# Optimization experiments

Hardware: AMD Instinct MI355X
Metric: run time of the kernel (lower is better)

## Reference

```python
import jax, jax.numpy as jnp
import numpy as np

EPS = 1e-4  # matches torch: x.norm(2, dim=1, keepdim=True) + 0.0001

def setup_inputs() -> dict:
    key = jax.random.key(0)
    k1, k2, k3 = jax.random.split(key, 3)
    B, IN, OUT = 16384, 2048, 2048
    x = jax.random.normal(k1, (B, IN), dtype=jnp.float32)
    # nn.Linear default init: U(-1/sqrt(in), 1/sqrt(in))
    bound = 1.0 / np.sqrt(IN)
    W = jax.random.uniform(k2, (OUT, IN), dtype=jnp.float32, minval=-bound, maxval=bound)
    b = jax.random.uniform(k3, (OUT,), dtype=jnp.float32, minval=-bound, maxval=bound)
    return {"x": x, "W": W, "b": b}

def reference(x, W, b):
    # L2-normalize each row, then Linear, then ReLU
    norm = jnp.linalg.norm(x, ord=2, axis=1, keepdims=True)  # [B, 1]
    x_dir = x / (norm + EPS)
    h = jnp.einsum('bi,oi->bo', x_dir, W) + b  # [B, OUT]
    return jax.nn.relu(h)
```

## Files before the change

kernel.cpp:

```cpp
#include <hip/hip_runtime.h>
#include <hip/hip_bf16.h>
#include <stdint.h>

#define B_ROWS 16384
#define IN_DIM 2048
#define OUT_DIM 2048

typedef __attribute__((ext_vector_type(4))) float f32x4;
typedef __attribute__((ext_vector_type(8))) short s16x8;

__device__ __forceinline__ unsigned short f2bf_rne(float f) {
  union { float f; unsigned u; } c; c.f = f;
  unsigned u = c.u;
  return (unsigned short)((u + 0x7FFFu + ((u >> 16) & 1u)) >> 16);
}

#define PREP_X_BLOCKS 4096
#define PREP_W_BLOCKS 2048

__global__ void __launch_bounds__(256) prep_kernel(const float* __restrict__ x,
                                                   unsigned short* __restrict__ xn,
                                                   float* __restrict__ scale,
                                                   const float* __restrict__ W,
                                                   unsigned short* __restrict__ Wb) {
  if (blockIdx.x < PREP_X_BLOCKS) {
    const int row  = (blockIdx.x * 256 + threadIdx.x) >> 6;
    const int lane = threadIdx.x & 63;
    const float4* xr = (const float4*)(x + (size_t)row * IN_DIM);
    unsigned short* xrow = xn + (size_t)row * IN_DIM;

    float ss = 0.0f;
    #pragma unroll
    for (int j = 0; j < 4; ++j) {
      const int f4 = j * 128 + lane * 2;
      float4 v0 = xr[f4 + 0];
      float4 v1 = xr[f4 + 1];
      ss += v0.x * v0.x + v0.y * v0.y + v0.z * v0.z + v0.w * v0.w +
            v1.x * v1.x + v1.y * v1.y + v1.z * v1.z + v1.w * v1.w;
      s16x8 p;
      p[0] = (short)f2bf_rne(v0.x); p[1] = (short)f2bf_rne(v0.y);
      p[2] = (short)f2bf_rne(v0.z); p[3] = (short)f2bf_rne(v0.w);
      p[4] = (short)f2bf_rne(v1.x); p[5] = (short)f2bf_rne(v1.y);
      p[6] = (short)f2bf_rne(v1.z); p[7] = (short)f2bf_rne(v1.w);
      *(s16x8*)(xrow + f4 * 4) = p;
    }

    #pragma unroll
    for (int m = 32; m > 0; m >>= 1) ss += __shfl_xor(ss, m, 64);
    if (lane == 0) scale[row] = 1.0f / (sqrtf(ss) + 1e-4f);
  } else {
    const size_t base = (size_t)(blockIdx.x - PREP_X_BLOCKS) * 2048 +
                        (size_t)threadIdx.x * 8;
    const float4* wp = (const float4*)(W + base);
    float4 v0 = wp[0];
    float4 v1 = wp[1];
    s16x8 p;
    p[0] = (short)f2bf_rne(v0.x); p[1] = (short)f2bf_rne(v0.y);
    p[2] = (short)f2bf_rne(v0.z); p[3] = (short)f2bf_rne(v0.w);
    p[4] = (short)f2bf_rne(v1.x); p[5] = (short)f2bf_rne(v1.y);
    p[6] = (short)f2bf_rne(v1.z); p[7] = (short)f2bf_rne(v1.w);
    *(s16x8*)(Wb + base) = p;
  }
}

__global__ void __launch_bounds__(256) gemm_kernel(const unsigned short* __restrict__ A,
                                                   const unsigned short* __restrict__ Bm,
                                                   const float* __restrict__ scale,
                                                   const float* __restrict__ bias,
                                                   float* __restrict__ out) {
  constexpr int BK = 64;
  __shared__ short As[128 * BK];
  __shared__ short Bs[128 * BK];

  const int tid = threadIdx.x;
  const int bid   = blockIdx.x;
  const int group = bid >> 7;
  const int w_    = bid & 127;
  const int bm    = group * 8 + (w_ & 7);
  const int bn    = w_ >> 3;

  const int lane = tid & 63;
  const int wave = tid >> 6;
  const int wm   = wave >> 1;
  const int wn   = wave & 1;
  const int lrow = lane & 15;
  const int lq   = lane >> 4;

  const int ar = tid >> 3;
  const int ac = ((tid & 7) ^ (ar & 7)) * 8;
  const unsigned short* ag = A  + (size_t)(bm * 128 + ar) * IN_DIM + ac;
  const unsigned short* bg = Bm + (size_t)(bn * 128 + ar) * IN_DIM + ac;
  char* asl = (char*)As + tid * 16;
  char* bsl = (char*)Bs + tid * 16;

  f32x4 acc[4][4] = {};

  for (int k0 = 0; k0 < IN_DIM; k0 += BK) {
    #pragma unroll
    for (int i = 0; i < 4; ++i) {
      __builtin_amdgcn_global_load_lds(
          (const __attribute__((address_space(1))) unsigned int*)(ag + (size_t)i * 32 * IN_DIM),
          (__attribute__((address_space(3))) unsigned int*)(asl + i * 4096), 16, 0, 0);
    }
    #pragma unroll
    for (int i = 0; i < 4; ++i) {
      __builtin_amdgcn_global_load_lds(
          (const __attribute__((address_space(1))) unsigned int*)(bg + (size_t)i * 32 * IN_DIM),
          (__attribute__((address_space(3))) unsigned int*)(bsl + i * 4096), 16, 0, 0);
    }
    ag += BK;
    bg += BK;
    __syncthreads();

    #pragma unroll
    for (int kk = 0; kk < 2; ++kk) {
      s16x8 af[4], bf[4];
      #pragma unroll
      for (int mi = 0; mi < 4; ++mi) {
        const int R = wm * 64 + mi * 16 + lrow;
        af[mi] = *(const s16x8*)(As + R * BK + (((kk * 4 + lq) ^ (lrow & 7)) * 8));
      }
      #pragma unroll
      for (int ni = 0; ni < 4; ++ni) {
        const int R = wn * 64 + ni * 16 + lrow;
        bf[ni] = *(const s16x8*)(Bs + R * BK + (((kk * 4 + lq) ^ (lrow & 7)) * 8));
      }
      #pragma unroll
      for (int mi = 0; mi < 4; ++mi)
        #pragma unroll
        for (int ni = 0; ni < 4; ++ni)
          acc[mi][ni] = __builtin_amdgcn_mfma_f32_16x16x32_bf16(af[mi], bf[ni], acc[mi][ni], 0, 0, 0);
    }
    __syncthreads();
  }

  const int row0 = bm * 128 + wm * 64 + lq * 4;
  const int col0 = bn * 128 + wn * 64 + lrow;
  #pragma unroll
  for (int mi = 0; mi < 4; ++mi) {
    const int row = row0 + mi * 16;
    const f32x4 sc = *(const f32x4*)(scale + row);
    #pragma unroll
    for (int ni = 0; ni < 4; ++ni) {
      const int col = col0 + ni * 16;
      const float bcol = bias[col];
      #pragma unroll
      for (int r = 0; r < 4; ++r) {
        float v = acc[mi][ni][r] * sc[r] + bcol;
        out[(size_t)(row + r) * OUT_DIM + col] = fmaxf(v, 0.0f);
      }
    }
  }
}

extern "C" void kernel_launch(void* const* d_in, const int* in_sizes, int n_in,
                              void* d_out, int out_size, void* d_ws, size_t ws_size,
                              hipStream_t stream) {
  const float* x = (const float*)d_in[0];
  const float* W = (const float*)d_in[1];
  const float* b = (const float*)d_in[2];
  float* out = (float*)d_out;

  char* ws = (char*)d_ws;
  unsigned short* xn    = (unsigned short*)ws;
  unsigned short* Wb    = (unsigned short*)(ws + (size_t)67108864);
  float*          scale = (float*)(ws + (size_t)67108864 + (size_t)8388608);

  prep_kernel<<<PREP_X_BLOCKS + PREP_W_BLOCKS, 256, 0, stream>>>(x, xn, scale, W, Wb);

  gemm_kernel<<<(OUT_DIM / 128) * (B_ROWS / 128), 256, 0, stream>>>(xn, Wb, scale, b, out);
}
```

Baseline: 374.2 us.

## Rewrite GEMM as 256x256 tile, double-buffered LDS, interleaved MFMA/load pipeline

Each GEMM block now computes a 256x256 tile with 512 threads (8 waves) instead of 128x128 with 256 threads. LDS is double-buffered so the next K-slice's global-to-LDS loads overlap MFMA work on the current slice, with finer barriers and s_setprio around the MFMA bursts. Block indices are remapped to follow the XCD layout so tiles that share data land on the same die. The larger tile raises arithmetic intensity and cuts LDS/global traffic per FLOP, at the cost of fewer blocks (512), more registers, 128KB of LDS and intricate vmcnt accounting that has to be exactly right.

New measurement: 363.3 us. 1.03x faster.

```diff
diff --git a/kernel.cpp b/kernel.cpp
--- a/kernel.cpp
+++ b/kernel.cpp
@@ -63,90 +63,155 @@
   }
 }
 
-__global__ void __launch_bounds__(256) gemm_kernel(const unsigned short* __restrict__ A,
-                                                   const unsigned short* __restrict__ Bm,
-                                                   const float* __restrict__ scale,
-                                                   const float* __restrict__ bias,
-                                                   float* __restrict__ out) {
-  constexpr int BK = 64;
-  __shared__ short As[128 * BK];
-  __shared__ short Bs[128 * BK];
+
+#define GLD16(SRC, DST)                                                        \
+  __builtin_amdgcn_global_load_lds(                                            \
+      (const __attribute__((address_space(1))) unsigned int*)(SRC),            \
+      (__attribute__((address_space(3))) unsigned int*)(DST), 16, 0, 0)
+
+__global__ void __launch_bounds__(512, 1) gemm_kernel(const unsigned short* __restrict__ A,
+                                                      const unsigned short* __restrict__ Bm,
+                                                      const float* __restrict__ scale,
+                                                      const float* __restrict__ bias,
+                                                      float* __restrict__ out) {
+  __shared__ unsigned short As[2][256 * 64];
+  __shared__ unsigned short Bs[2][256 * 64];
 
   const int tid = threadIdx.x;
-  const int bid   = blockIdx.x;
-  const int group = bid >> 7;
-  const int w_    = bid & 127;
-  const int bm    = group * 8 + (w_ & 7);
-  const int bn    = w_ >> 3;
+  const int bid = blockIdx.x;
+  const int xcd = bid & 7;
+  const int loc = bid >> 3;
+  const int bm  = xcd * 8 + (loc >> 3);
+  const int bn  = loc & 7;
 
   const int lane = tid & 63;
   const int wave = tid >> 6;
-  const int wm   = wave >> 1;
-  const int wn   = wave & 1;
+  const int wm   = wave >> 2;
+  const int wn   = wave & 3;
   const int lrow = lane & 15;
   const int lq   = lane >> 4;
 
-  const int ar = tid >> 3;
-  const int ac = ((tid & 7) ^ (ar & 7)) * 8;
-  const unsigned short* ag = A  + (size_t)(bm * 128 + ar) * IN_DIM + ac;
-  const unsigned short* bg = Bm + (size_t)(bn * 128 + ar) * IN_DIM + ac;
-  char* asl = (char*)As + tid * 16;
-  char* bsl = (char*)Bs + tid * 16;
-
-  f32x4 acc[4][4] = {};
-
-  for (int k0 = 0; k0 < IN_DIM; k0 += BK) {
-    #pragma unroll
-    for (int i = 0; i < 4; ++i) {
-      __builtin_amdgcn_global_load_lds(
-          (const __attribute__((address_space(1))) unsigned int*)(ag + (size_t)i * 32 * IN_DIM),
-          (__attribute__((address_space(3))) unsigned int*)(asl + i * 4096), 16, 0, 0);
+  const int sr = tid >> 3;
+  const int sc = tid & 7;
+  const unsigned short* aG = A  + (size_t)(bm * 256 + sr) * IN_DIM + ((sc ^ (sr & 7)) * 8);
+  const unsigned short* bG = Bm + (size_t)(bn * 256 + sr) * IN_DIM + ((sc ^ (sr & 7)) * 8);
+
+  const int aRow = (wm * 128 + lrow) * 64;
+  const int bRow = (wn * 64  + lrow) * 64;
+  const int c0   = (lq ^ (lrow & 7)) * 8;
+
+  f32x4 acc[8][4] = {};
+  s16x8 af[4] = {};
+  s16x8 bf[4][2] = {};
+
+  {
+    char* aD = (char*)&As[0][0] + tid * 16;
+    char* bD = (char*)&Bs[0][0] + tid * 16;
+    GLD16(bG,                         bD);
+    GLD16(bG + (size_t) 64 * IN_DIM,  bD + 8192);
+    GLD16(bG + (size_t)128 * IN_DIM,  bD + 16384);
+    GLD16(bG + (size_t)192 * IN_DIM,  bD + 24576);
+    GLD16(aG,                         aD);
+    GLD16(aG + (size_t)128 * IN_DIM,  aD + 16384);
+    GLD16(aG + (size_t) 64 * IN_DIM,  aD + 8192);
+    GLD16(aG + (size_t)192 * IN_DIM,  aD + 24576);
+  }
+  asm volatile("s_waitcnt vmcnt(2)" ::: "memory");
+  __builtin_amdgcn_s_barrier();
+
+  for (int T = 0; T < IN_DIM / 64; ++T) {
+    const int cur = T & 1, nxt = cur ^ 1;
+    const size_t kN = (size_t)((T < IN_DIM / 64 - 1) ? (T + 1) * 64 : 0);
+    char* aD = (char*)&As[nxt][0] + tid * 16;
+    char* bD = (char*)&Bs[nxt][0] + tid * 16;
+    const unsigned short* aS = aG + kN;
+    const unsigned short* bS = bG + kN;
+
+    __builtin_amdgcn_s_setprio(1);
+    #pragma unroll
+    for (int mi = 0; mi < 4; ++mi)
+      #pragma unroll
+      for (int ni = 0; ni < 4; ++ni)
+        acc[4 + mi][ni] = __builtin_amdgcn_mfma_f32_16x16x32_bf16(af[mi], bf[ni][1], acc[4 + mi][ni], 0, 0, 0);
+    __builtin_amdgcn_s_setprio(0);
+    #pragma unroll
+    for (int ni = 0; ni < 4; ++ni) {
+      bf[ni][0] = *(const s16x8*)(&Bs[cur][bRow + ni * 1024 + c0]);
+      bf[ni][1] = *(const s16x8*)(&Bs[cur][bRow + ni * 1024 + (c0 ^ 32)]);
     }
     #pragma unroll
-    for (int i = 0; i < 4; ++i) {
-      __builtin_amdgcn_global_load_lds(
-          (const __attribute__((address_space(1))) unsigned int*)(bg + (size_t)i * 32 * IN_DIM),
-          (__attribute__((address_space(3))) unsigned int*)(bsl + i * 4096), 16, 0, 0);
-    }
-    ag += BK;
-    bg += BK;
-    __syncthreads();
-
-    #pragma unroll
-    for (int kk = 0; kk < 2; ++kk) {
-      s16x8 af[4], bf[4];
-      #pragma unroll
-      for (int mi = 0; mi < 4; ++mi) {
-        const int R = wm * 64 + mi * 16 + lrow;
-        af[mi] = *(const s16x8*)(As + R * BK + (((kk * 4 + lq) ^ (lrow & 7)) * 8));
-      }
-      #pragma unroll
-      for (int ni = 0; ni < 4; ++ni) {
-        const int R = wn * 64 + ni * 16 + lrow;
-        bf[ni] = *(const s16x8*)(Bs + R * BK + (((kk * 4 + lq) ^ (lrow & 7)) * 8));
-      }
-      #pragma unroll
-      for (int mi = 0; mi < 4; ++mi)
-        #pragma unroll
-        for (int ni = 0; ni < 4; ++ni)
-          acc[mi][ni] = __builtin_amdgcn_mfma_f32_16x16x32_bf16(af[mi], bf[ni], acc[mi][ni], 0, 0, 0);
-    }
-    __syncthreads();
-  }
-
-  const int row0 = bm * 128 + wm * 64 + lq * 4;
-  const int col0 = bn * 128 + wn * 64 + lrow;
+    for (int mi = 0; mi < 4; ++mi)
+      af[mi] = *(const s16x8*)(&As[cur][aRow + mi * 1024 + c0]);
+    GLD16(bS,                        bD);
+    GLD16(bS + (size_t)64 * IN_DIM,  bD + 8192);
+    __builtin_amdgcn_s_barrier();
+
+    __builtin_amdgcn_s_setprio(1);
+    #pragma unroll
+    for (int mi = 0; mi < 4; ++mi)
+      #pragma unroll
+      for (int ni = 0; ni < 4; ++ni)
+        acc[mi][ni] = __builtin_amdgcn_mfma_f32_16x16x32_bf16(af[mi], bf[ni][0], acc[mi][ni], 0, 0, 0);
+    __builtin_amdgcn_s_setprio(0);
+    #pragma unroll
+    for (int mi = 0; mi < 4; ++mi)
+      af[mi] = *(const s16x8*)(&As[cur][aRow + mi * 1024 + (c0 ^ 32)]);
+    GLD16(bS + (size_t)128 * IN_DIM, bD + 16384);
+    GLD16(bS + (size_t)192 * IN_DIM, bD + 24576);
+    asm volatile("s_waitcnt vmcnt(4)" ::: "memory");
+    __builtin_amdgcn_s_barrier();
+
+    __builtin_amdgcn_s_setprio(1);
+    #pragma unroll
+    for (int mi = 0; mi < 4; ++mi)
+      #pragma unroll
+      for (int ni = 0; ni < 4; ++ni)
+        acc[mi][ni] = __builtin_amdgcn_mfma_f32_16x16x32_bf16(af[mi], bf[ni][1], acc[mi][ni], 0, 0, 0);
+    __builtin_amdgcn_s_setprio(0);
+    #pragma unroll
+    for (int mi = 0; mi < 4; ++mi)
+      af[mi] = *(const s16x8*)(&As[cur][aRow + (4 + mi) * 1024 + c0]);
+    GLD16(aS,                        aD);
+    GLD16(aS + (size_t)128 * IN_DIM, aD + 16384);
+    __builtin_amdgcn_s_barrier();
+
+    __builtin_amdgcn_s_setprio(1);
+    #pragma unroll
+    for (int mi = 0; mi < 4; ++mi)
+      #pragma unroll
+      for (int ni = 0; ni < 4; ++ni)
+        acc[4 + mi][ni] = __builtin_amdgcn_mfma_f32_16x16x32_bf16(af[mi], bf[ni][0], acc[4 + mi][ni], 0, 0, 0);
+    __builtin_amdgcn_s_setprio(0);
+    #pragma unroll
+    for (int mi = 0; mi < 4; ++mi)
+      af[mi] = *(const s16x8*)(&As[cur][aRow + (4 + mi) * 1024 + (c0 ^ 32)]);
+    GLD16(aS + (size_t)64  * IN_DIM, aD + 8192);
+    GLD16(aS + (size_t)192 * IN_DIM, aD + 24576);
+    asm volatile("s_waitcnt vmcnt(2)" ::: "memory");
+    __builtin_amdgcn_s_barrier();
+  }
+
+  __builtin_amdgcn_s_setprio(1);
   #pragma unroll
-  for (int mi = 0; mi < 4; ++mi) {
+  for (int mi = 0; mi < 4; ++mi)
+    #pragma unroll
+    for (int ni = 0; ni < 4; ++ni)
+      acc[4 + mi][ni] = __builtin_amdgcn_mfma_f32_16x16x32_bf16(af[mi], bf[ni][1], acc[4 + mi][ni], 0, 0, 0);
+  __builtin_amdgcn_s_setprio(0);
+
+  const int row0 = bm * 256 + wm * 128 + lq * 4;
+  const int col0 = bn * 256 + wn * 64 + lrow;
+  #pragma unroll
+  for (int mi = 0; mi < 8; ++mi) {
     const int row = row0 + mi * 16;
-    const f32x4 sc = *(const f32x4*)(scale + row);
+    const f32x4 sc4 = *(const f32x4*)(scale + row);
     #pragma unroll
     for (int ni = 0; ni < 4; ++ni) {
       const int col = col0 + ni * 16;
       const float bcol = bias[col];
       #pragma unroll
       for (int r = 0; r < 4; ++r) {
-        float v = acc[mi][ni][r] * sc[r] + bcol;
+        float v = acc[mi][ni][r] * sc4[r] + bcol;
         out[(size_t)(row + r) * OUT_DIM + col] = fmaxf(v, 0.0f);
       }
     }
@@ -168,5 +233,5 @@
 
   prep_kernel<<<PREP_X_BLOCKS + PREP_W_BLOCKS, 256, 0, stream>>>(x, xn, scale, W, Wb);
 
-  gemm_kernel<<<(OUT_DIM / 128) * (B_ROWS / 128), 256, 0, stream>>>(xn, Wb, scale, b, out);
-}
+  gemm_kernel<<<(OUT_DIM / 256) * (B_ROWS / 256), 512, 0, stream>>>(xn, Wb, scale, b, out);
+}
```

## Rewrite GEMM as 256x256 tile, 8-wave, double-buffered ping-pong pipeline

Applied to the files above, without the earlier changes.

The GEMM kernel moves from 128x128 tiles with 4 waves to 256x256 tiles with 8 waves. It double-buffers LDS in half-tiles, and the direct global-to-LDS loads for the next K slices are interleaved with MFMA phases using explicit waitcnt, barriers and setprio. Block-to-tile mapping changes to an XCD-aware swizzle so each XCD works on neighbouring M rows. The aim is to hide global load latency and raise arithmetic intensity per block. In exchange it uses 128KB of LDS, forcing one block per CU, and relies on hand-tuned wait counts that are fragile.

Result: faster. 360.5 us (-3.7%).

```diff
diff --git a/kernel.cpp b/kernel.cpp
--- a/kernel.cpp
+++ b/kernel.cpp
@@ -63,90 +63,182 @@
   }
 }
 
-__global__ void __launch_bounds__(256) gemm_kernel(const unsigned short* __restrict__ A,
-                                                   const unsigned short* __restrict__ Bm,
-                                                   const float* __restrict__ scale,
-                                                   const float* __restrict__ bias,
-                                                   float* __restrict__ out) {
-  constexpr int BK = 64;
-  __shared__ short As[128 * BK];
-  __shared__ short Bs[128 * BK];
+
+#define GLD16(SRC, DST)                                                        \
+  __builtin_amdgcn_global_load_lds(                                            \
+      (const __attribute__((address_space(1))) unsigned int*)(SRC),            \
+      (__attribute__((address_space(3))) unsigned int*)(DST), 16, 0, 0)
+
+#define STAGE_A(par, h, kofs) do {                                             \
+    char* d_ = (char*)&As[par][h][0] + tid * 16;                               \
+    GLD16(aG + (kofs) + (size_t)((h) * 64) * IN_DIM,       d_);                \
+    GLD16(aG + (kofs) + (size_t)((h) * 64 + 128) * IN_DIM, d_ + 8192);         \
+  } while (0)
+
+#define STAGE_B(par, h, kofs) do {                                             \
+    char* d_ = (char*)&Bs[par][h][0] + tid * 16;                               \
+    const unsigned short* s_ = (h) ? bG1 : bG0;                                \
+    GLD16(s_ + (kofs),                          d_);                           \
+    GLD16(s_ + (kofs) + (size_t)128 * IN_DIM,   d_ + 8192);                    \
+  } while (0)
+
+#define READ_A(par, mh) do {                                                   \
+    _Pragma("unroll") for (int mi = 0; mi < 4; ++mi) {                         \
+      af[mi][0] = *(const s16x8*)(&As[par][mh][aOff + mi * 1024 + c0]);        \
+      af[mi][1] = *(const s16x8*)(&As[par][mh][aOff + mi * 1024 + (c0 ^ 32)]); \
+    } } while (0)
+
+#define READ_B(par, nh, dst) do {                                              \
+    _Pragma("unroll") for (int ni = 0; ni < 2; ++ni) {                         \
+      dst[ni][0] = *(const s16x8*)(&Bs[par][nh][bOff + ni * 1024 + c0]);       \
+      dst[ni][1] = *(const s16x8*)(&Bs[par][nh][bOff + ni * 1024 + (c0 ^ 32)]);\
+    } } while (0)
+
+#define MFMA16(mh, nh, bfr) do {                                               \
+    __builtin_amdgcn_s_setprio(1);                                             \
+    _Pragma("unroll") for (int kk = 0; kk < 2; ++kk)                           \
+    _Pragma("unroll") for (int mi = 0; mi < 4; ++mi)                           \
+    _Pragma("unroll") for (int ni = 0; ni < 2; ++ni)                           \
+      acc[(mh) * 4 + mi][(nh) * 2 + ni] =                                      \
+          __builtin_amdgcn_mfma_f32_16x16x32_bf16(                             \
+              af[mi][kk], bfr[ni][kk], acc[(mh) * 4 + mi][(nh) * 2 + ni],      \
+              0, 0, 0);                                                        \
+    __builtin_amdgcn_s_setprio(0);                                             \
+  } while (0)
+
+#define BAR()     __builtin_amdgcn_s_barrier()
+#define SCHED0()  __builtin_amdgcn_sched_barrier(0)
+#define LGKM0()   do { asm volatile("s_waitcnt lgkmcnt(0)" ::: "memory"); SCHED0(); } while (0)
+#define LGKM8()   asm volatile("s_waitcnt lgkmcnt(8)" ::: "memory")
+#define VM6()     asm volatile("s_waitcnt vmcnt(6)" ::: "memory")
+
+__global__ void __launch_bounds__(512, 1) gemm_kernel(const unsigned short* __restrict__ A,
+                                                      const unsigned short* __restrict__ Bm,
+                                                      const float* __restrict__ scale,
+                                                      const float* __restrict__ bias,
+                                                      float* __restrict__ out) {
+  __shared__ unsigned short As[2][2][128 * 64];
+  __shared__ unsigned short Bs[2][2][128 * 64];
 
   const int tid = threadIdx.x;
-  const int bid   = blockIdx.x;
-  const int group = bid >> 7;
-  const int w_    = bid & 127;
-  const int bm    = group * 8 + (w_ & 7);
-  const int bn    = w_ >> 3;
+  const int bid = blockIdx.x;
+  const int xcd = bid & 7;
+  const int loc = bid >> 3;
+  const int bm  = xcd * 8 + (loc >> 3);
+  const int bn  = loc & 7;
 
   const int lane = tid & 63;
   const int wave = tid >> 6;
-  const int wm   = wave >> 1;
-  const int wn   = wave & 1;
+  const int wm   = wave >> 2;
+  const int wn   = wave & 3;
   const int lrow = lane & 15;
   const int lq   = lane >> 4;
 
-  const int ar = tid >> 3;
-  const int ac = ((tid & 7) ^ (ar & 7)) * 8;
-  const unsigned short* ag = A  + (size_t)(bm * 128 + ar) * IN_DIM + ac;
-  const unsigned short* bg = Bm + (size_t)(bn * 128 + ar) * IN_DIM + ac;
-  char* asl = (char*)As + tid * 16;
-  char* bsl = (char*)Bs + tid * 16;
-
-  f32x4 acc[4][4] = {};
-
-  for (int k0 = 0; k0 < IN_DIM; k0 += BK) {
+  const int sr = tid >> 3;
+  const int sc = tid & 7;
+  const size_t swz = (size_t)((sc ^ (sr & 7)) * 8);
+  const unsigned short* aG  = A  + (size_t)(bm * 256 + sr) * IN_DIM + swz;
+  const unsigned short* bG0 = Bm + (size_t)(bn * 256 + (sr >> 5) * 64 + (sr & 31)) * IN_DIM + swz;
+  const unsigned short* bG1 = bG0 + (size_t)32 * IN_DIM;
+
+  const int aOff = (wm * 64 + lrow) * 64;
+  const int bOff = (wn * 32 + lrow) * 64;
+  const int c0   = (lq ^ (lrow & 7)) * 8;
+
+  f32x4 acc[8][4] = {};
+  s16x8 af[4][2], b0[2][2], b1[2][2];
+
+  STAGE_A(0, 0, (size_t)0);
+  STAGE_B(0, 0, (size_t)0);
+  STAGE_B(0, 1, (size_t)0);
+  STAGE_A(0, 1, (size_t)0);
+  STAGE_A(1, 0, (size_t)64);
+  STAGE_B(1, 0, (size_t)64);
+  STAGE_B(1, 1, (size_t)64);
+  VM6();
+  BAR();
+  SCHED0();
+
+  #pragma unroll 1
+  for (int i = 0; i < 16; ++i) {
+    const size_t kP1 = (size_t)(2 * i + 1) * 64;
+    const size_t kT2 = (i < 15) ? (size_t)(2 * i + 2) * 64 : 0;
+    const size_t kT3 = (i < 15) ? (size_t)(2 * i + 3) * 64 : 0;
+
+    READ_A(0, 0);
+    READ_B(0, 0, b0);
+    STAGE_A(1, 1, kP1);
+    LGKM8();
+    BAR();
+    LGKM0();
+    MFMA16(0, 0, b0);
+    BAR(); SCHED0();
+
+    READ_B(0, 1, b1);
+    STAGE_A(0, 0, kT2);
+    BAR();
+    LGKM0();
+    MFMA16(0, 1, b1);
+    BAR(); SCHED0();
+
+    READ_A(0, 1);
+    STAGE_B(0, 0, kT2);
+    BAR();
+    LGKM0();
+    MFMA16(1, 0, b0);
+    BAR(); SCHED0();
+
+    STAGE_B(0, 1, kT2);
+    BAR();
+    MFMA16(1, 1, b1);
+    VM6();
+    BAR(); SCHED0();
+
+    READ_A(1, 0);
+    READ_B(1, 0, b0);
+    STAGE_A(0, 1, kT2);
+    LGKM8();
+    BAR();
+    LGKM0();
+    MFMA16(0, 0, b0);
+    BAR(); SCHED0();
+
+    READ_B(1, 1, b1);
+    STAGE_A(1, 0, kT3);
+    BAR();
+    LGKM0();
+    MFMA16(0, 1, b1);
+    BAR(); SCHED0();
+
+    READ_A(1, 1);
+    STAGE_B(1, 0, kT3);
+    BAR();
+    LGKM0();
+    MFMA16(1, 0, b0);
+    BAR(); SCHED0();
+
+    STAGE_B(1, 1, kT3);
+    BAR();
+    MFMA16(1, 1, b1);
+    VM6();
+    BAR(); SCHED0();
+  }
+
+  asm volatile("s_waitcnt vmcnt(0)" ::: "memory");
+
+  const int row0 = bm * 256 + wm * 128 + lq * 4;
+  const int col0 = bn * 256 + wn * 64 + lrow;
+  #pragma unroll
+  for (int a = 0; a < 8; ++a) {
+    const int row = row0 + (a >> 2) * 64 + (a & 3) * 16;
+    const f32x4 sc4 = *(const f32x4*)(scale + row);
     #pragma unroll
-    for (int i = 0; i < 4; ++i) {
-      __builtin_amdgcn_global_load_lds(
-          (const __attribute__((address_space(1))) unsigned int*)(ag + (size_t)i * 32 * IN_DIM),
-          (__attribute__((address_space(3))) unsigned int*)(asl + i * 4096), 16, 0, 0);
-    }
-    #pragma unroll
-    for (int i = 0; i < 4; ++i) {
-      __builtin_amdgcn_global_load_lds(
-          (const __attribute__((address_space(1))) unsigned int*)(bg + (size_t)i * 32 * IN_DIM),
-          (__attribute__((address_space(3))) unsigned int*)(bsl + i * 4096), 16, 0, 0);
-    }
-    ag += BK;
-    bg += BK;
-    __syncthreads();
-
-    #pragma unroll
-    for (int kk = 0; kk < 2; ++kk) {
-      s16x8 af[4], bf[4];
-      #pragma unroll
-      for (int mi = 0; mi < 4; ++mi) {
-        const int R = wm * 64 + mi * 16 + lrow;
-        af[mi] = *(const s16x8*)(As + R * BK + (((kk * 4 + lq) ^ (lrow & 7)) * 8));
-      }
-      #pragma unroll
-      for (int ni = 0; ni < 4; ++ni) {
-        const int R = wn * 64 + ni * 16 + lrow;
-        bf[ni] = *(const s16x8*)(Bs + R * BK + (((kk * 4 + lq) ^ (lrow & 7)) * 8));
-      }
-      #pragma unroll
-      for (int mi = 0; mi < 4; ++mi)
-        #pragma unroll
-        for (int ni = 0; ni < 4; ++ni)
-          acc[mi][ni] = __builtin_amdgcn_mfma_f32_16x16x32_bf16(af[mi], bf[ni], acc[mi][ni], 0, 0, 0);
-    }
-    __syncthreads();
-  }
-
-  const int row0 = bm * 128 + wm * 64 + lq * 4;
-  const int col0 = bn * 128 + wn * 64 + lrow;
-  #pragma unroll
-  for (int mi = 0; mi < 4; ++mi) {
-    const int row = row0 + mi * 16;
-    const f32x4 sc = *(const f32x4*)(scale + row);
-    #pragma unroll
-    for (int ni = 0; ni < 4; ++ni) {
-      const int col = col0 + ni * 16;
+    for (int b2 = 0; b2 < 4; ++b2) {
+      const int col = col0 + (b2 >> 1) * 32 + (b2 & 1) * 16;
       const float bcol = bias[col];
       #pragma unroll
       for (int r = 0; r < 4; ++r) {
-        float v = acc[mi][ni][r] * sc[r] + bcol;
+        float v = acc[a][b2][r] * sc4[r] + bcol;
         out[(size_t)(row + r) * OUT_DIM + col] = fmaxf(v, 0.0f);
       }
     }
@@ -168,5 +260,5 @@
 
   prep_kernel<<<PREP_X_BLOCKS + PREP_W_BLOCKS, 256, 0, stream>>>(x, xn, scale, W, Wb);
 
-  gemm_kernel<<<(OUT_DIM / 128) * (B_ROWS / 128), 256, 0, stream>>>(xn, Wb, scale, b, out);
-}
+  gemm_kernel<<<(OUT_DIM / 256) * (B_ROWS / 256), 512, 0, stream>>>(xn, Wb, scale, b, out);
+}
```

## Double-buffer GEMM LDS tiles, remap blocks per XCD, and recoalesce prep loads

Applied to the files above, without the earlier changes.

Moves the GEMM main loop to double-buffered LDS. The next K tile is issued with global_load_lds while MFMAs run on the current one, which drops one barrier per iteration. Block indices are remapped so each XCD handles a contiguous band of row tiles, intended to improve L2 reuse. The MFMA section is wrapped in s_setprio, and launch bounds request two blocks per CU. The prep kernel switches to per-lane contiguous 16-byte float4 loads with fma accumulation. Costs are double the LDS (64KB per block), which may limit occupancy. The last iteration also redundantly prefetches tile 0.

After: 388.7 us. +3.9%, slower.

```diff
diff --git a/kernel.cpp b/kernel.cpp
--- a/kernel.cpp
+++ b/kernel.cpp
@@ -8,6 +8,7 @@
 
 typedef __attribute__((ext_vector_type(4))) float f32x4;
 typedef __attribute__((ext_vector_type(8))) short s16x8;
+typedef __attribute__((ext_vector_type(4))) unsigned short u16x4;
 
 __device__ __forceinline__ unsigned short f2bf_rne(float f) {
   union { float f; unsigned u; } c; c.f = f;
@@ -26,58 +27,63 @@
   if (blockIdx.x < PREP_X_BLOCKS) {
     const int row  = (blockIdx.x * 256 + threadIdx.x) >> 6;
     const int lane = threadIdx.x & 63;
-    const float4* xr = (const float4*)(x + (size_t)row * IN_DIM);
-    unsigned short* xrow = xn + (size_t)row * IN_DIM;
+    const f32x4* xr = (const f32x4*)(x + (size_t)row * IN_DIM);
+    u16x4* xw = (u16x4*)(xn + (size_t)row * IN_DIM);
 
     float ss = 0.0f;
     #pragma unroll
-    for (int j = 0; j < 4; ++j) {
-      const int f4 = j * 128 + lane * 2;
-      float4 v0 = xr[f4 + 0];
-      float4 v1 = xr[f4 + 1];
-      ss += v0.x * v0.x + v0.y * v0.y + v0.z * v0.z + v0.w * v0.w +
-            v1.x * v1.x + v1.y * v1.y + v1.z * v1.z + v1.w * v1.w;
-      s16x8 p;
-      p[0] = (short)f2bf_rne(v0.x); p[1] = (short)f2bf_rne(v0.y);
-      p[2] = (short)f2bf_rne(v0.z); p[3] = (short)f2bf_rne(v0.w);
-      p[4] = (short)f2bf_rne(v1.x); p[5] = (short)f2bf_rne(v1.y);
-      p[6] = (short)f2bf_rne(v1.z); p[7] = (short)f2bf_rne(v1.w);
-      *(s16x8*)(xrow + f4 * 4) = p;
+    for (int j = 0; j < 8; ++j) {
+      const int i = j * 64 + lane;
+      f32x4 v = xr[i];
+      ss = fmaf(v[0], v[0], ss);
+      ss = fmaf(v[1], v[1], ss);
+      ss = fmaf(v[2], v[2], ss);
+      ss = fmaf(v[3], v[3], ss);
+      u16x4 p;
+      p[0] = f2bf_rne(v[0]); p[1] = f2bf_rne(v[1]);
+      p[2] = f2bf_rne(v[2]); p[3] = f2bf_rne(v[3]);
+      xw[i] = p;
     }
 
     #pragma unroll
     for (int m = 32; m > 0; m >>= 1) ss += __shfl_xor(ss, m, 64);
     if (lane == 0) scale[row] = 1.0f / (sqrtf(ss) + 1e-4f);
   } else {
-    const size_t base = (size_t)(blockIdx.x - PREP_X_BLOCKS) * 2048 +
-                        (size_t)threadIdx.x * 8;
-    const float4* wp = (const float4*)(W + base);
-    float4 v0 = wp[0];
-    float4 v1 = wp[1];
-    s16x8 p;
-    p[0] = (short)f2bf_rne(v0.x); p[1] = (short)f2bf_rne(v0.y);
-    p[2] = (short)f2bf_rne(v0.z); p[3] = (short)f2bf_rne(v0.w);
-    p[4] = (short)f2bf_rne(v1.x); p[5] = (short)f2bf_rne(v1.y);
-    p[6] = (short)f2bf_rne(v1.z); p[7] = (short)f2bf_rne(v1.w);
-    *(s16x8*)(Wb + base) = p;
+    const int base = (blockIdx.x - PREP_X_BLOCKS) * 512 + threadIdx.x;
+    const f32x4* wr = (const f32x4*)W;
+    u16x4* ww = (u16x4*)Wb;
+    #pragma unroll
+    for (int j = 0; j < 2; ++j) {
+      const int i = base + j * 256;
+      f32x4 v = wr[i];
+      u16x4 p;
+      p[0] = f2bf_rne(v[0]); p[1] = f2bf_rne(v[1]);
+      p[2] = f2bf_rne(v[2]); p[3] = f2bf_rne(v[3]);
+      ww[i] = p;
+    }
   }
 }
 
-__global__ void __launch_bounds__(256) gemm_kernel(const unsigned short* __restrict__ A,
-                                                   const unsigned short* __restrict__ Bm,
-                                                   const float* __restrict__ scale,
-                                                   const float* __restrict__ bias,
-                                                   float* __restrict__ out) {
-  constexpr int BK = 64;
-  __shared__ short As[128 * BK];
-  __shared__ short Bs[128 * BK];
+
+#define GLD16(SRC, DST)                                                        \
+  __builtin_amdgcn_global_load_lds(                                            \
+      (const __attribute__((address_space(1))) unsigned int*)(SRC),            \
+      (__attribute__((address_space(3))) unsigned int*)(DST), 16, 0, 0)
+
+__global__ void __launch_bounds__(256, 2) gemm_kernel(const unsigned short* __restrict__ A,
+                                                      const unsigned short* __restrict__ Bm,
+                                                      const float* __restrict__ scale,
+                                                      const float* __restrict__ bias,
+                                                      float* __restrict__ out) {
+  __shared__ unsigned short As[2][128 * 64];
+  __shared__ unsigned short Bs[2][128 * 64];
 
   const int tid = threadIdx.x;
-  const int bid   = blockIdx.x;
-  const int group = bid >> 7;
-  const int w_    = bid & 127;
-  const int bm    = group * 8 + (w_ & 7);
-  const int bn    = w_ >> 3;
+  const int bid = blockIdx.x;
+  const int xcd = bid & 7;
+  const int loc = bid >> 3;
+  const int bm  = xcd * 16 + (loc >> 4);
+  const int bn  = loc & 15;
 
   const int lane = tid & 63;
   const int wave = tid >> 6;
@@ -86,51 +92,63 @@
   const int lrow = lane & 15;
   const int lq   = lane >> 4;
 
-  const int ar = tid >> 3;
-  const int ac = ((tid & 7) ^ (ar & 7)) * 8;
-  const unsigned short* ag = A  + (size_t)(bm * 128 + ar) * IN_DIM + ac;
-  const unsigned short* bg = Bm + (size_t)(bn * 128 + ar) * IN_DIM + ac;
-  char* asl = (char*)As + tid * 16;
-  char* bsl = (char*)Bs + tid * 16;
+  const int sr = tid >> 3;
+  const int sc = tid & 7;
+  const unsigned short* aG = A  + (size_t)(bm * 128 + sr) * IN_DIM + ((sc ^ (sr & 7)) * 8);
+  const unsigned short* bG = Bm + (size_t)(bn * 128 + sr) * IN_DIM + ((sc ^ (sr & 7)) * 8);
+
+  const int aRow = (wm * 64 + lrow) * 64;
+  const int bRow = (wn * 64 + lrow) * 64;
+  const int c0   = (lq ^ (lrow & 7)) * 8;
 
   f32x4 acc[4][4] = {};
 
-  for (int k0 = 0; k0 < IN_DIM; k0 += BK) {
+  {
+    char* aD = (char*)&As[0][0] + tid * 16;
+    char* bD = (char*)&Bs[0][0] + tid * 16;
     #pragma unroll
     for (int i = 0; i < 4; ++i) {
-      __builtin_amdgcn_global_load_lds(
-          (const __attribute__((address_space(1))) unsigned int*)(ag + (size_t)i * 32 * IN_DIM),
-          (__attribute__((address_space(3))) unsigned int*)(asl + i * 4096), 16, 0, 0);
+      GLD16(aG + (size_t)(i * 32) * IN_DIM, aD + i * 4096);
+      GLD16(bG + (size_t)(i * 32) * IN_DIM, bD + i * 4096);
     }
-    #pragma unroll
-    for (int i = 0; i < 4; ++i) {
-      __builtin_amdgcn_global_load_lds(
-          (const __attribute__((address_space(1))) unsigned int*)(bg + (size_t)i * 32 * IN_DIM),
-          (__attribute__((address_space(3))) unsigned int*)(bsl + i * 4096), 16, 0, 0);
+  }
+  __syncthreads();
+
+  for (int T = 0; T < IN_DIM / 64; ++T) {
+    const int cur = T & 1, nxt = cur ^ 1;
+    const size_t kN = (size_t)((T < 31) ? (T + 1) * 64 : 0);
+
+    {
+      char* aD = (char*)&As[nxt][0] + tid * 16;
+      char* bD = (char*)&Bs[nxt][0] + tid * 16;
+      #pragma unroll
+      for (int i = 0; i < 4; ++i) {
+        GLD16(aG + kN + (size_t)(i * 32) * IN_DIM, aD + i * 4096);
+        GLD16(bG + kN + (size_t)(i * 32) * IN_DIM, bD + i * 4096);
+      }
     }
-    ag += BK;
-    bg += BK;
-    __syncthreads();
 
+    const unsigned short* Ac = &As[cur][0];
+    const unsigned short* Bc = &Bs[cur][0];
     #pragma unroll
     for (int kk = 0; kk < 2; ++kk) {
+      const int ck = c0 ^ (kk * 32);
       s16x8 af[4], bf[4];
       #pragma unroll
-      for (int mi = 0; mi < 4; ++mi) {
-        const int R = wm * 64 + mi * 16 + lrow;
-        af[mi] = *(const s16x8*)(As + R * BK + (((kk * 4 + lq) ^ (lrow & 7)) * 8));
-      }
+      for (int mi = 0; mi < 4; ++mi)
+        af[mi] = *(const s16x8*)(Ac + aRow + mi * 1024 + ck);
       #pragma unroll
-      for (int ni = 0; ni < 4; ++ni) {
-        const int R = wn * 64 + ni * 16 + lrow;
-        bf[ni] = *(const s16x8*)(Bs + R * BK + (((kk * 4 + lq) ^ (lrow & 7)) * 8));
-      }
+      for (int ni = 0; ni < 4; ++ni)
+        bf[ni] = *(const s16x8*)(Bc + bRow + ni * 1024 + ck);
+      __builtin_amdgcn_s_setprio(1);
       #pragma unroll
       for (int mi = 0; mi < 4; ++mi)
         #pragma unroll
         for (int ni = 0; ni < 4; ++ni)
           acc[mi][ni] = __builtin_amdgcn_mfma_f32_16x16x32_bf16(af[mi], bf[ni], acc[mi][ni], 0, 0, 0);
+      __builtin_amdgcn_s_setprio(0);
     }
+
     __syncthreads();
   }
 
@@ -139,14 +157,14 @@
   #pragma unroll
   for (int mi = 0; mi < 4; ++mi) {
     const int row = row0 + mi * 16;
-    const f32x4 sc = *(const f32x4*)(scale + row);
+    const f32x4 sc4 = *(const f32x4*)(scale + row);
     #pragma unroll
     for (int ni = 0; ni < 4; ++ni) {
       const int col = col0 + ni * 16;
       const float bcol = bias[col];
       #pragma unroll
       for (int r = 0; r < 4; ++r) {
-        float v = acc[mi][ni][r] * sc[r] + bcol;
+        float v = acc[mi][ni][r] * sc4[r] + bcol;
         out[(size_t)(row + r) * OUT_DIM + col] = fmaxf(v, 0.0f);
       }
     }
```
